# Kernel optimization log

Measured on AMD Instinct MI355X. Metric: run time of the kernel, lower is better.

The kernel has to match this reference:

```python
import jax, jax.numpy as jnp
import numpy as np

C_IN = 128
C_OUT = 128
P = 3
V = 4096
FIFO_SIZE = 17  # 2*kernel_size - 1, kernel_size = 9


def setup_inputs() -> dict:
    key = jax.random.key(0)
    k1, k2, k3, k4 = jax.random.split(key, 4)
    x = jax.random.normal(k1, (1, C_IN, V, 1), dtype=jnp.float32)
    A = jax.random.uniform(k2, (P, V, V), dtype=jnp.float32) / V  # roughly normalized adjacency
    fifo = jax.random.normal(k3, (FIFO_SIZE, P, C_OUT, V), dtype=jnp.float32)
    W = jax.random.normal(k4, (P * C_OUT, C_IN), dtype=jnp.float32) * 0.02  # 1x1 conv weight
    b = jnp.zeros((P * C_OUT,), dtype=jnp.float32)
    return {"x": x, "A": A, "fifo": fifo, "W": W, "b": b}


def reference(x, A, fifo, W, b):
    # x: (1, C_in, V, 1) single graph frame; residual = identity (C_in == C_out, stride 1)
    xv = x[0, :, :, 0]                                   # (C_in, V)
    # 1x1 conv -> split into P partitions: (P, C_out, V)
    z = (W @ xv + b[:, None]).reshape(P, C_OUT, V)
    # per-partition adjacency matmul: (P, C_out, V) @ (P, V, V)
    d = jnp.einsum('pcv,pvw->pcw', z, A)
    # FIFO push: newest frame in front, drop oldest
    new_fifo = jnp.concatenate([d[None], fifo[:FIFO_SIZE - 1]], axis=0)  # (FIFO, P, C_out, V)
    # temporal + partition reduction
    e = new_fifo.sum(axis=(0, 1))                        # (C_out, V)
    out = jax.nn.relu(e + xv)[None]                      # (1, C_out, V)
    return out
```

## Files before the change

### kernel.cpp

```cpp
#include <hip/hip_runtime.h>

typedef float f32x4 __attribute__((ext_vector_type(4)));
typedef __bf16 bf16x8 __attribute__((ext_vector_type(8)));

constexpr int V = 4096;

__device__ __forceinline__ unsigned short f2bf(float f) {
    unsigned int u = __float_as_uint(f);
    u += 0x7FFFu + ((u >> 16) & 1u);
    return (unsigned short)(u >> 16);
}

__global__ __launch_bounds__(256) void k_z(const float* __restrict__ x,
                                           const float* __restrict__ W,
                                           const float* __restrict__ b,
                                           unsigned short* __restrict__ zb) {
    __shared__ float Ws[8 * 128];
    __shared__ float bs[8];
    const int rg = blockIdx.x;
    const int vb = blockIdx.y;
    const int t  = threadIdx.x;
    reinterpret_cast<f32x4*>(Ws)[t] = reinterpret_cast<const f32x4*>(W + rg * 1024)[t];
    if (t < 8) bs[t] = b[rg * 8 + t];
    __syncthreads();
    const int v = vb * 256 + t;
    float acc[8] = {};
    for (int j = 0; j < 128; ++j) {
        const float xj = x[j * V + v];
        #pragma unroll
        for (int q = 0; q < 8; ++q) acc[q] = fmaf(Ws[q * 128 + j], xj, acc[q]);
    }
    #pragma unroll
    for (int q = 0; q < 8; ++q)
        zb[(size_t)(rg * 8 + q) * V + v] = f2bf(acc[q] + bs[q]);
}

__global__ __launch_bounds__(256) void k_gemm(const unsigned short* __restrict__ zb,
                                              const float* __restrict__ A,
                                              float* __restrict__ partial) {
    __shared__ unsigned short Bt[32][72];
    const int nt = blockIdx.x;
    const int p  = blockIdx.y;
    const int kh = blockIdx.z;
    const int n0 = nt * 32;
    const int kbase = kh * 2048;
    const int t    = threadIdx.x;
    const int wid  = t >> 6;
    const int lane = t & 63;
    const int lrow = lane & 15;
    const int g    = lane >> 4;

    const float* Ap = A + (size_t)p * V * V;
    const unsigned short* Zw = zb + ((size_t)p * 128 + wid * 32) * V;

    const int kk = t >> 2;
    const int c4 = t & 3;

    f32x4 acc00 = {}, acc01 = {}, acc10 = {}, acc11 = {};

    for (int k0 = kbase; k0 < kbase + 2048; k0 += 64) {
        const float* src = Ap + (size_t)(k0 + kk) * V + n0 + c4 * 4;
        f32x4 av0 = *reinterpret_cast<const f32x4*>(src);
        f32x4 av1 = *reinterpret_cast<const f32x4*>(src + 16);
        __syncthreads();
        #pragma unroll
        for (int j = 0; j < 4; ++j) {
            Bt[c4 * 4 + j][kk]      = f2bf(av0[j]);
            Bt[16 + c4 * 4 + j][kk] = f2bf(av1[j]);
        }
        __syncthreads();
        const unsigned short* zrow = Zw + (size_t)lrow * V + k0 + g * 8;
        #pragma unroll
        for (int ks = 0; ks < 2; ++ks) {
            bf16x8 b0 = *reinterpret_cast<const bf16x8*>(&Bt[lrow][ks * 32 + g * 8]);
            bf16x8 b1 = *reinterpret_cast<const bf16x8*>(&Bt[16 + lrow][ks * 32 + g * 8]);
            bf16x8 a0 = *reinterpret_cast<const bf16x8*>(zrow + ks * 32);
            bf16x8 a1 = *reinterpret_cast<const bf16x8*>(zrow + (size_t)16 * V + ks * 32);
            acc00 = __builtin_amdgcn_mfma_f32_16x16x32_bf16(a0, b0, acc00, 0, 0, 0);
            acc01 = __builtin_amdgcn_mfma_f32_16x16x32_bf16(a0, b1, acc01, 0, 0, 0);
            acc10 = __builtin_amdgcn_mfma_f32_16x16x32_bf16(a1, b0, acc10, 0, 0, 0);
            acc11 = __builtin_amdgcn_mfma_f32_16x16x32_bf16(a1, b1, acc11, 0, 0, 0);
        }
    }

    float* Pp = partial + (size_t)(p * 2 + kh) * 128 * V;
    #pragma unroll
    for (int r = 0; r < 4; ++r) {
        const int m0 = wid * 32 + g * 4 + r;
        Pp[(size_t)m0 * V + n0 + lrow]             = acc00[r];
        Pp[(size_t)m0 * V + n0 + 16 + lrow]        = acc01[r];
        Pp[(size_t)(m0 + 16) * V + n0 + lrow]      = acc10[r];
        Pp[(size_t)(m0 + 16) * V + n0 + 16 + lrow] = acc11[r];
    }
}

__global__ __launch_bounds__(256) void k_epi(const float* __restrict__ x,
                                             const float* __restrict__ fifo,
                                             const float* __restrict__ partial,
                                             float* __restrict__ out) {
    const size_t off  = ((size_t)blockIdx.x * 256 + threadIdx.x) * 4;
    const size_t slab = (size_t)128 * V;
    f32x4 s0 = *reinterpret_cast<const f32x4*>(x + off);
    f32x4 s1 = {}, s2 = {}, s3 = {};
    #pragma unroll
    for (int q = 0; q < 6; ++q) {
        f32x4 pv = *reinterpret_cast<const f32x4*>(partial + (size_t)q * slab + off);
        if (q & 1) s1 += pv; else s2 += pv;
    }
    #pragma unroll
    for (int s = 0; s < 48; ++s) {
        f32x4 fv = *reinterpret_cast<const f32x4*>(fifo + (size_t)s * slab + off);
        switch (s & 3) {
            case 0: s0 += fv; break;
            case 1: s1 += fv; break;
            case 2: s2 += fv; break;
            default: s3 += fv; break;
        }
    }
    f32x4 sum = (s0 + s1) + (s2 + s3);
    f32x4 o;
    #pragma unroll
    for (int j = 0; j < 4; ++j) o[j] = fmaxf(sum[j], 0.0f);
    *reinterpret_cast<f32x4*>(out + off) = o;
}

extern "C" void kernel_launch(void* const* d_in, const int* in_sizes, int n_in,
                              void* d_out, int out_size, void* d_ws, size_t ws_size,
                              hipStream_t stream) {
    const float* x    = (const float*)d_in[0];
    const float* A    = (const float*)d_in[1];
    const float* fifo = (const float*)d_in[2];
    const float* W    = (const float*)d_in[3];
    const float* b    = (const float*)d_in[4];
    float* out = (float*)d_out;

    unsigned short* zb = (unsigned short*)d_ws;
    float* partial = (float*)((char*)d_ws + (size_t)384 * V * 2);

    k_z   <<<dim3(48, 16),   256, 0, stream>>>(x, W, b, zb);
    k_gemm<<<dim3(128, 3, 2), 256, 0, stream>>>(zb, A, partial);
    k_epi <<<dim3(512),       256, 0, stream>>>(x, fifo, partial, out);
}
```

Baseline: 104.9 us.

## Software-pipeline A and z loads with double-buffered LDS in gemm; vectorize z kernel

The gemm kernel now double-buffers the shared-memory B tile and prefetches the next A tile and z fragments into registers one iteration ahead, so global-load latency overlaps with MFMA work. The loop is unrolled by two phases, with clamped prefetch indices at the tail. The k_z kernel is vectorized to process four columns per thread with float4 loads and packed bf16 stores, and its grid is cut to a quarter. These changes raise register pressure, and the z kernel has fewer blocks, which may lower occupancy.

```diff
diff --git a/kernel.cpp b/kernel.cpp
--- a/kernel.cpp
+++ b/kernel.cpp
@@ -2,6 +2,7 @@
 
 typedef float f32x4 __attribute__((ext_vector_type(4)));
 typedef __bf16 bf16x8 __attribute__((ext_vector_type(8)));
+typedef unsigned short u16x4 __attribute__((ext_vector_type(4)));
 
 constexpr int V = 4096;
 
@@ -23,27 +24,32 @@
     reinterpret_cast<f32x4*>(Ws)[t] = reinterpret_cast<const f32x4*>(W + rg * 1024)[t];
     if (t < 8) bs[t] = b[rg * 8 + t];
     __syncthreads();
-    const int v = vb * 256 + t;
-    float acc[8] = {};
+    const int v = vb * 1024 + t * 4;
+    f32x4 acc[8] = {};
+    #pragma unroll 8
     for (int j = 0; j < 128; ++j) {
-        const float xj = x[j * V + v];
+        f32x4 xv = *reinterpret_cast<const f32x4*>(x + (size_t)j * V + v);
         #pragma unroll
-        for (int q = 0; q < 8; ++q) acc[q] = fmaf(Ws[q * 128 + j], xj, acc[q]);
+        for (int q = 0; q < 8; ++q) acc[q] += Ws[q * 128 + j] * xv;
     }
     #pragma unroll
-    for (int q = 0; q < 8; ++q)
-        zb[(size_t)(rg * 8 + q) * V + v] = f2bf(acc[q] + bs[q]);
+    for (int q = 0; q < 8; ++q) {
+        u16x4 u;
+        #pragma unroll
+        for (int j = 0; j < 4; ++j) u[j] = f2bf(acc[q][j] + bs[q]);
+        *reinterpret_cast<u16x4*>(zb + (size_t)(rg * 8 + q) * V + v) = u;
+    }
 }
 
 __global__ __launch_bounds__(256) void k_gemm(const unsigned short* __restrict__ zb,
                                               const float* __restrict__ A,
                                               float* __restrict__ partial) {
-    __shared__ unsigned short Bt[32][72];
+    __shared__ unsigned short Bt[2][32][72];
     const int nt = blockIdx.x;
     const int p  = blockIdx.y;
     const int kh = blockIdx.z;
     const int n0 = nt * 32;
-    const int kbase = kh * 2048;
+    const int kbase = kh * 2048, kend = kbase + 2048;
     const int t    = threadIdx.x;
     const int wid  = t >> 6;
     const int lane = t & 63;
@@ -51,36 +57,67 @@
     const int g    = lane >> 4;
 
     const float* Ap = A + (size_t)p * V * V;
-    const unsigned short* Zw = zb + ((size_t)p * 128 + wid * 32) * V;
+    const unsigned short* Zw = zb + ((size_t)p * 128 + wid * 32) * V + (size_t)lrow * V + g * 8;
 
     const int kk = t >> 2;
     const int c4 = t & 3;
 
     f32x4 acc00 = {}, acc01 = {}, acc10 = {}, acc11 = {};
+    f32x4 aA0, aA1, aB0, aB1;
+    bf16x8 zA0, zA1, zA2, zA3, zB0, zB1, zB2, zB3;
 
-    for (int k0 = kbase; k0 < kbase + 2048; k0 += 64) {
-        const float* src = Ap + (size_t)(k0 + kk) * V + n0 + c4 * 4;
-        f32x4 av0 = *reinterpret_cast<const f32x4*>(src);
-        f32x4 av1 = *reinterpret_cast<const f32x4*>(src + 16);
+#define LOADA(d0, d1, K) { const float* s_ = Ap + (size_t)((K) + kk) * V + n0 + c4 * 4; \
+        d0 = *reinterpret_cast<const f32x4*>(s_); \
+        d1 = *reinterpret_cast<const f32x4*>(s_ + 16); }
+
+#define LOADZ(z0_, z1_, z2_, z3_, K) { const unsigned short* zr_ = Zw + (K); \
+        z0_ = *reinterpret_cast<const bf16x8*>(zr_); \
+        z1_ = *reinterpret_cast<const bf16x8*>(zr_ + (size_t)16 * V); \
+        z2_ = *reinterpret_cast<const bf16x8*>(zr_ + 32); \
+        z3_ = *reinterpret_cast<const bf16x8*>(zr_ + (size_t)16 * V + 32); }
+
+#define WRITELDS(B, a0, a1) { \
+        Bt[B][c4 * 4 + 0][kk] = f2bf(a0[0]); Bt[B][c4 * 4 + 1][kk] = f2bf(a0[1]); \
+        Bt[B][c4 * 4 + 2][kk] = f2bf(a0[2]); Bt[B][c4 * 4 + 3][kk] = f2bf(a0[3]); \
+        Bt[B][16 + c4 * 4 + 0][kk] = f2bf(a1[0]); Bt[B][16 + c4 * 4 + 1][kk] = f2bf(a1[1]); \
+        Bt[B][16 + c4 * 4 + 2][kk] = f2bf(a1[2]); Bt[B][16 + c4 * 4 + 3][kk] = f2bf(a1[3]); }
+
+#define MFMA_PHASE(B, zz0, zz1, zz2, zz3) { \
+        bf16x8 b0l = *reinterpret_cast<const bf16x8*>(&Bt[B][lrow][g * 8]); \
+        bf16x8 b1l = *reinterpret_cast<const bf16x8*>(&Bt[B][16 + lrow][g * 8]); \
+        bf16x8 b0h = *reinterpret_cast<const bf16x8*>(&Bt[B][lrow][32 + g * 8]); \
+        bf16x8 b1h = *reinterpret_cast<const bf16x8*>(&Bt[B][16 + lrow][32 + g * 8]); \
+        acc00 = __builtin_amdgcn_mfma_f32_16x16x32_bf16(zz0, b0l, acc00, 0, 0, 0); \
+        acc01 = __builtin_amdgcn_mfma_f32_16x16x32_bf16(zz0, b1l, acc01, 0, 0, 0); \
+        acc10 = __builtin_amdgcn_mfma_f32_16x16x32_bf16(zz1, b0l, acc10, 0, 0, 0); \
+        acc11 = __builtin_amdgcn_mfma_f32_16x16x32_bf16(zz1, b1l, acc11, 0, 0, 0); \
+        acc00 = __builtin_amdgcn_mfma_f32_16x16x32_bf16(zz2, b0h, acc00, 0, 0, 0); \
+        acc01 = __builtin_amdgcn_mfma_f32_16x16x32_bf16(zz2, b1h, acc01, 0, 0, 0); \
+        acc10 = __builtin_amdgcn_mfma_f32_16x16x32_bf16(zz3, b0h, acc10, 0, 0, 0); \
+        acc11 = __builtin_amdgcn_mfma_f32_16x16x32_bf16(zz3, b1h, acc11, 0, 0, 0); }
+
+    LOADA(aA0, aA1, kbase);
+    LOADA(aB0, aB1, kbase + 64);
+    LOADZ(zA0, zA1, zA2, zA3, kbase);
+
+    for (int k0 = kbase; k0 < kend; k0 += 128) {
+        const int kA = (k0 + 128 < kend) ? k0 + 128 : kend - 64;
+        const int kB = (k0 + 192 < kend) ? k0 + 192 : kend - 64;
+        const int kZ = (k0 + 128 < kend) ? k0 + 128 : kbase;
+
         __syncthreads();
-        #pragma unroll
-        for (int j = 0; j < 4; ++j) {
-            Bt[c4 * 4 + j][kk]      = f2bf(av0[j]);
-            Bt[16 + c4 * 4 + j][kk] = f2bf(av1[j]);
-        }
+        WRITELDS(0, aA0, aA1);
         __syncthreads();
-        const unsigned short* zrow = Zw + (size_t)lrow * V + k0 + g * 8;
-        #pragma unroll
-        for (int ks = 0; ks < 2; ++ks) {
-            bf16x8 b0 = *reinterpret_cast<const bf16x8*>(&Bt[lrow][ks * 32 + g * 8]);
-            bf16x8 b1 = *reinterpret_cast<const bf16x8*>(&Bt[16 + lrow][ks * 32 + g * 8]);
-            bf16x8 a0 = *reinterpret_cast<const bf16x8*>(zrow + ks * 32);
-            bf16x8 a1 = *reinterpret_cast<const bf16x8*>(zrow + (size_t)16 * V + ks * 32);
-            acc00 = __builtin_amdgcn_mfma_f32_16x16x32_bf16(a0, b0, acc00, 0, 0, 0);
-            acc01 = __builtin_amdgcn_mfma_f32_16x16x32_bf16(a0, b1, acc01, 0, 0, 0);
-            acc10 = __builtin_amdgcn_mfma_f32_16x16x32_bf16(a1, b0, acc10, 0, 0, 0);
-            acc11 = __builtin_amdgcn_mfma_f32_16x16x32_bf16(a1, b1, acc11, 0, 0, 0);
-        }
+        LOADA(aA0, aA1, kA);
+        LOADZ(zB0, zB1, zB2, zB3, k0 + 64);
+        MFMA_PHASE(0, zA0, zA1, zA2, zA3);
+
+        __syncthreads();
+        WRITELDS(1, aB0, aB1);
+        __syncthreads();
+        LOADA(aB0, aB1, kB);
+        LOADZ(zA0, zA1, zA2, zA3, kZ);
+        MFMA_PHASE(1, zB0, zB1, zB2, zB3);
     }
 
     float* Pp = partial + (size_t)(p * 2 + kh) * 128 * V;
@@ -92,6 +129,10 @@
         Pp[(size_t)(m0 + 16) * V + n0 + lrow]      = acc10[r];
         Pp[(size_t)(m0 + 16) * V + n0 + 16 + lrow] = acc11[r];
     }
+#undef LOADA
+#undef LOADZ
+#undef WRITELDS
+#undef MFMA_PHASE
 }
 
 __global__ __launch_bounds__(256) void k_epi(const float* __restrict__ x,
@@ -137,7 +178,7 @@
     unsigned short* zb = (unsigned short*)d_ws;
     float* partial = (float*)((char*)d_ws + (size_t)384 * V * 2);
 
-    k_z   <<<dim3(48, 16),   256, 0, stream>>>(x, W, b, zb);
+    k_z   <<<dim3(48, 4),     256, 0, stream>>>(x, W, b, zb);
     k_gemm<<<dim3(128, 3, 2), 256, 0, stream>>>(zb, A, partial);
     k_epi <<<dim3(512),       256, 0, stream>>>(x, fifo, partial, out);
 }
```

Result: slower. 115.2 us (+9.9%).

## Overlap FIFO reduction with adjacency GEMM via interleaved blocks; vectorize z kernel

Applied to the files above, without the earlier changes.

Folds the 48-slab FIFO sum (plus x residual) into the GEMM launch: every seventh block does the FIFO reduction into a workspace buffer while the others run the bf16 MFMA GEMM. The bandwidth-bound FIFO read can then overlap with the A-streaming GEMM, and the final epilogue only reads the partials and the precomputed sum. The z kernel is also vectorized to process four columns per thread with 8-byte bf16 stores. The cost is an extra fsum write and read, plus mixed block types competing for bandwidth within one launch.

```diff
diff --git a/kernel.cpp b/kernel.cpp
--- a/kernel.cpp
+++ b/kernel.cpp
@@ -2,6 +2,7 @@
 
 typedef float f32x4 __attribute__((ext_vector_type(4)));
 typedef __bf16 bf16x8 __attribute__((ext_vector_type(8)));
+typedef unsigned short u16x4 __attribute__((ext_vector_type(4)));
 
 constexpr int V = 4096;
 
@@ -23,28 +24,69 @@
     reinterpret_cast<f32x4*>(Ws)[t] = reinterpret_cast<const f32x4*>(W + rg * 1024)[t];
     if (t < 8) bs[t] = b[rg * 8 + t];
     __syncthreads();
-    const int v = vb * 256 + t;
-    float acc[8] = {};
+    const int v = vb * 1024 + t * 4;
+    f32x4 acc[8] = {};
+    #pragma unroll 8
     for (int j = 0; j < 128; ++j) {
-        const float xj = x[j * V + v];
+        f32x4 xv = *reinterpret_cast<const f32x4*>(x + (size_t)j * V + v);
         #pragma unroll
-        for (int q = 0; q < 8; ++q) acc[q] = fmaf(Ws[q * 128 + j], xj, acc[q]);
+        for (int q = 0; q < 8; ++q) acc[q] += Ws[q * 128 + j] * xv;
     }
     #pragma unroll
-    for (int q = 0; q < 8; ++q)
-        zb[(size_t)(rg * 8 + q) * V + v] = f2bf(acc[q] + bs[q]);
+    for (int q = 0; q < 8; ++q) {
+        u16x4 u;
+        #pragma unroll
+        for (int j = 0; j < 4; ++j) u[j] = f2bf(acc[q][j] + bs[q]);
+        *reinterpret_cast<u16x4*>(zb + (size_t)(rg * 8 + q) * V + v) = u;
+    }
 }
 
-__global__ __launch_bounds__(256) void k_gemm(const unsigned short* __restrict__ zb,
-                                              const float* __restrict__ A,
-                                              float* __restrict__ partial) {
+__global__ __launch_bounds__(256) void k_fused(const unsigned short* __restrict__ zb,
+                                               const float* __restrict__ A,
+                                               const float* __restrict__ x,
+                                               const float* __restrict__ fifo,
+                                               float* __restrict__ partial,
+                                               float* __restrict__ fsum) {
     __shared__ unsigned short Bt[32][72];
-    const int nt = blockIdx.x;
-    const int p  = blockIdx.y;
-    const int kh = blockIdx.z;
+    const int bid = blockIdx.x;
+    const int t   = threadIdx.x;
+
+    if (bid % 7 == 3) {
+        const int rid = bid / 7;
+        const size_t off  = (size_t)rid * 4096 + (size_t)t * 16;
+        const size_t slab = (size_t)128 * V;
+        f32x4 e0 = *reinterpret_cast<const f32x4*>(x + off);
+        f32x4 e1 = *reinterpret_cast<const f32x4*>(x + off + 4);
+        f32x4 e2 = *reinterpret_cast<const f32x4*>(x + off + 8);
+        f32x4 e3 = *reinterpret_cast<const f32x4*>(x + off + 12);
+        f32x4 o0 = {}, o1 = {}, o2 = {}, o3 = {};
+        #pragma unroll
+        for (int s = 0; s < 48; s += 2) {
+            const float* f0 = fifo + (size_t)s * slab + off;
+            const float* f1 = fifo + (size_t)(s + 1) * slab + off;
+            e0 += *reinterpret_cast<const f32x4*>(f0);
+            e1 += *reinterpret_cast<const f32x4*>(f0 + 4);
+            e2 += *reinterpret_cast<const f32x4*>(f0 + 8);
+            e3 += *reinterpret_cast<const f32x4*>(f0 + 12);
+            o0 += *reinterpret_cast<const f32x4*>(f1);
+            o1 += *reinterpret_cast<const f32x4*>(f1 + 4);
+            o2 += *reinterpret_cast<const f32x4*>(f1 + 8);
+            o3 += *reinterpret_cast<const f32x4*>(f1 + 12);
+        }
+        *reinterpret_cast<f32x4*>(fsum + off)      = e0 + o0;
+        *reinterpret_cast<f32x4*>(fsum + off + 4)  = e1 + o1;
+        *reinterpret_cast<f32x4*>(fsum + off + 8)  = e2 + o2;
+        *reinterpret_cast<f32x4*>(fsum + off + 12) = e3 + o3;
+        return;
+    }
+
+    const int aid = bid - (bid + 3) / 7;
+    const int nt  = aid & 127;
+    const int pk  = aid >> 7;
+    const int p   = pk >> 1;
+    const int kh  = pk & 1;
     const int n0 = nt * 32;
     const int kbase = kh * 2048;
-    const int t    = threadIdx.x;
     const int wid  = t >> 6;
     const int lane = t & 63;
     const int lrow = lane & 15;
@@ -83,7 +125,7 @@
         }
     }
 
-    float* Pp = partial + (size_t)(p * 2 + kh) * 128 * V;
+    float* Pp = partial + (size_t)pk * 128 * V;
     #pragma unroll
     for (int r = 0; r < 4; ++r) {
         const int m0 = wid * 32 + g * 4 + r;
@@ -94,30 +136,19 @@
     }
 }
 
-__global__ __launch_bounds__(256) void k_epi(const float* __restrict__ x,
-                                             const float* __restrict__ fifo,
-                                             const float* __restrict__ partial,
-                                             float* __restrict__ out) {
+__global__ __launch_bounds__(256) void k_epi2(const float* __restrict__ partial,
+                                              const float* __restrict__ fsum,
+                                              float* __restrict__ out) {
     const size_t off  = ((size_t)blockIdx.x * 256 + threadIdx.x) * 4;
     const size_t slab = (size_t)128 * V;
-    f32x4 s0 = *reinterpret_cast<const f32x4*>(x + off);
-    f32x4 s1 = {}, s2 = {}, s3 = {};
+    f32x4 s0 = *reinterpret_cast<const f32x4*>(fsum + off);
+    f32x4 s1 = {};
     #pragma unroll
     for (int q = 0; q < 6; ++q) {
         f32x4 pv = *reinterpret_cast<const f32x4*>(partial + (size_t)q * slab + off);
-        if (q & 1) s1 += pv; else s2 += pv;
+        if (q & 1) s1 += pv; else s0 += pv;
     }
-    #pragma unroll
-    for (int s = 0; s < 48; ++s) {
-        f32x4 fv = *reinterpret_cast<const f32x4*>(fifo + (size_t)s * slab + off);
-        switch (s & 3) {
-            case 0: s0 += fv; break;
-            case 1: s1 += fv; break;
-            case 2: s2 += fv; break;
-            default: s3 += fv; break;
-        }
-    }
-    f32x4 sum = (s0 + s1) + (s2 + s3);
+    f32x4 sum = s0 + s1;
     f32x4 o;
     #pragma unroll
     for (int j = 0; j < 4; ++j) o[j] = fmaxf(sum[j], 0.0f);
@@ -135,9 +166,10 @@
     float* out = (float*)d_out;
 
     unsigned short* zb = (unsigned short*)d_ws;
-    float* partial = (float*)((char*)d_ws + (size_t)384 * V * 2);
+    float* partial = (float*)((char*)d_ws + (size_t)3 * 1024 * 1024);
+    float* fsum    = (float*)((char*)d_ws + (size_t)15 * 1024 * 1024);
 
-    k_z   <<<dim3(48, 16),   256, 0, stream>>>(x, W, b, zb);
-    k_gemm<<<dim3(128, 3, 2), 256, 0, stream>>>(zb, A, partial);
-    k_epi <<<dim3(512),       256, 0, stream>>>(x, fifo, partial, out);
+    k_z    <<<dim3(48, 4), 256, 0, stream>>>(x, W, b, zb);
+    k_fused<<<dim3(896),   256, 0, stream>>>(zb, A, x, fifo, partial, fsum);
+    k_epi2 <<<dim3(512),   256, 0, stream>>>(partial, fsum, out);
 }
```

New measurement: 146.1 us. 1.39x slower.
